# Optimization experiments

Hardware: AMD Instinct MI355X
Metric: run time of the kernel (lower is better)

The kernel has to match this reference:

```python
import jax, jax.numpy as jnp
import numpy as np

KS = 2          # kernel_size
THRESH = 0.0    # conv filter threshold
D = 64          # embed_dim


def setup_inputs() -> dict:
    key = jax.random.key(0)
    k1, k2 = jax.random.split(key, 2)
    x = jax.random.normal(k1, (8, 1, 65, 65), dtype=jnp.float32)
    proj_w = jax.random.normal(k2, (1, D), dtype=jnp.float32) / jnp.sqrt(jnp.float32(D))
    proj_b = jnp.zeros((1,), dtype=jnp.float32)
    return {"x": x, "proj_w": proj_w, "proj_b": proj_b}


def reference(x, proj_w, proj_b):
    B = x.shape[0]
    # non-overlapping stride-1 unfold -> patches (B, KS*KS, H', W')
    patches = jax.lax.conv_general_dilated_patches(x, (KS, KS), (1, 1), 'VALID')
    pat = patches.reshape(B, KS * KS, -1)            # (B, kk, N)
    # Conv.run: one scalar per patch index, shared across the batch
    scalar = jnp.tanh(jnp.mean(pat, axis=(0, 1)) - THRESH)  # (N,)
    N = scalar.shape[0]
    conv_out = jnp.broadcast_to(scalar, (B, N))      # (B, N)
    # np.tile of conv scalar across embed_dim
    embed = jnp.broadcast_to(conv_out[..., None], (B, N, D))  # (B, N, D)
    # rotation/entangle params are identity matrices -> Q = K = V = embed
    scores = jnp.einsum('bnd,bmd->bnm', embed, embed) / jnp.sqrt(jnp.float32(D))
    attn = jax.nn.softmax(scores, axis=-1)           # (B, N, N)
    ctx = jnp.einsum('bnm,bmd->bnd', attn, embed)    # (B, N, D)
    pooled = ctx.mean(axis=1)                        # (B, D)
    out = pooled @ proj_w.T + proj_b                 # (B, 1)
    return out[:, 0]
```

## Files before the change

### kernel.cpp

```cpp
#include <hip/hip_runtime.h>

#define NROW 4096
#define NCOL 4225
#define BATCH 8
#define MAGIC 0x13579BDFu


__device__ __forceinline__ float fast_tanh(float x) {
    float e = __builtin_exp2f(2.885390082f * x);
    return 1.0f - 2.0f / (e + 1.0f);
}

__global__ void __launch_bounds__(1024) k_fused(const float* __restrict__ x,
                                                const float* __restrict__ proj_w,
                                                const float* __restrict__ proj_b,
                                                float* __restrict__ out,
                                                float* __restrict__ partial,
                                                unsigned* __restrict__ flags) {
    __shared__ __align__(16) float cs_sh[NCOL];
    __shared__ __align__(16) float s_sh[NROW];
    __shared__ float c_sh[16];
    const int tid = threadIdx.x;
    const int bid = blockIdx.x;

#pragma unroll
    for (int k = 0; k < 4; ++k) {
        int p = tid + (k << 10);
        float v = 0.0f;
#pragma unroll
        for (int b = 0; b < BATCH; ++b) v += x[b * NCOL + p];
        cs_sh[p] = v;
    }
    if (tid < NCOL - NROW) {
        int p = NROW + tid;
        float v = 0.0f;
#pragma unroll
        for (int b = 0; b < BATCH; ++b) v += x[b * NCOL + p];
        cs_sh[p] = v;
    }
    __syncthreads();

#pragma unroll
    for (int k = 0; k < 4; ++k) {
        int n = tid + (k << 10);
        int i = n >> 6, j = n & 63;
        const float* c = &cs_sh[i * 65 + j];
        s_sh[n] = fast_tanh((c[0] + c[1] + c[65] + c[66]) * (1.0f / 32.0f));
    }
    __syncthreads();

    const int wave = tid >> 6;
    const int lane = tid & 63;
    const int row = (bid << 4) + wave;
    const float t = 8.0f * 1.4426950408889634f * s_sh[row];
    float num = 0.0f, den = 0.0f;
    const float4* s4 = (const float4*)s_sh;
#pragma unroll
    for (int k = 0; k < 16; ++k) {
        float4 sv = s4[lane + (k << 6)];
        float e0 = __builtin_exp2f(t * sv.x);
        float e1 = __builtin_exp2f(t * sv.y);
        float e2 = __builtin_exp2f(t * sv.z);
        float e3 = __builtin_exp2f(t * sv.w);
        num += e0 * sv.x;
        den += e0;
        num += e1 * sv.y;
        den += e1;
        num += e2 * sv.z;
        den += e2;
        num += e3 * sv.w;
        den += e3;
    }
#pragma unroll
    for (int off = 32; off; off >>= 1) {
        num += __shfl_down(num, off, 64);
        den += __shfl_down(den, off, 64);
    }
    if (lane == 0) c_sh[wave] = num / den;
    __syncthreads();

    if (tid == 0) {
        float bs = 0.0f;
#pragma unroll
        for (int r = 0; r < 16; ++r) bs += c_sh[r];
        atomicExch(&partial[bid], bs);
        __threadfence();
        atomicExch(&flags[bid], MAGIC);
    }

    if (bid == 0 && tid < 64) {
        float pw = proj_w[tid];
        float pb = proj_b[0];
#pragma unroll
        for (int q = 0; q < 4; ++q) {
            int i = tid + (q << 6);
            while (atomicAdd(&flags[i], 0u) != MAGIC) __builtin_amdgcn_s_sleep(1);
        }
        __threadfence();
        float acc_c = 0.0f;
#pragma unroll
        for (int q = 0; q < 4; ++q) {
            int i = tid + (q << 6);
            acc_c += atomicAdd(&partial[i], 0.0f);
        }
#pragma unroll
        for (int off = 32; off; off >>= 1) {
            acc_c += __shfl_down(acc_c, off, 64);
            pw    += __shfl_down(pw, off, 64);
        }
        if (tid == 0) {
            float o = (acc_c * (1.0f / (float)NROW)) * pw + pb;
#pragma unroll
            for (int b = 0; b < BATCH; ++b) out[b] = o;
        }
    }
}

extern "C" void kernel_launch(void* const* d_in, const int* in_sizes, int n_in,
                              void* d_out, int out_size, void* d_ws, size_t ws_size,
                              hipStream_t stream) {
    const float* x      = (const float*)d_in[0];
    const float* proj_w = (const float*)d_in[1];
    const float* proj_b = (const float*)d_in[2];
    float* out = (float*)d_out;

    float*    partial = (float*)d_ws;
    unsigned* flags   = (unsigned*)(partial + 256);

    k_fused<<<256, 1024, 0, stream>>>(x, proj_w, proj_b, out, partial, flags);
}
```

Before: 67.84 us.

## Replace in-kernel flag spin synchronisation with a separate final reduction kernel

Splits the fused kernel into a per-row kernel that writes one partial sum per block and a tiny one-wave kernel that reduces the partials and applies the projection. This removes the atomic flag publishing, the fences and the spin-wait in block 0, which also removes the reliance on flags that were never reset between calls. The cost is an extra kernel launch and the dependency gap between the two kernels on the stream.

```diff
diff --git a/kernel.cpp b/kernel.cpp
--- a/kernel.cpp
+++ b/kernel.cpp
@@ -3,7 +3,6 @@
 #define NROW 4096
 #define NCOL 4225
 #define BATCH 8
-#define MAGIC 0x13579BDFu
 
 
 __device__ __forceinline__ float fast_tanh(float x) {
@@ -11,12 +10,8 @@
     return 1.0f - 2.0f / (e + 1.0f);
 }
 
-__global__ void __launch_bounds__(1024) k_fused(const float* __restrict__ x,
-                                                const float* __restrict__ proj_w,
-                                                const float* __restrict__ proj_b,
-                                                float* __restrict__ out,
-                                                float* __restrict__ partial,
-                                                unsigned* __restrict__ flags) {
+__global__ void __launch_bounds__(1024) k_rows(const float* __restrict__ x,
+                                               float* __restrict__ partial) {
     __shared__ __align__(16) float cs_sh[NCOL];
     __shared__ __align__(16) float s_sh[NROW];
     __shared__ float c_sh[16];
@@ -83,36 +78,28 @@
         float bs = 0.0f;
 #pragma unroll
         for (int r = 0; r < 16; ++r) bs += c_sh[r];
-        atomicExch(&partial[bid], bs);
-        __threadfence();
-        atomicExch(&flags[bid], MAGIC);
+        partial[bid] = bs;
     }
+}
 
-    if (bid == 0 && tid < 64) {
-        float pw = proj_w[tid];
-        float pb = proj_b[0];
+__global__ void __launch_bounds__(64) k_final(const float* __restrict__ partial,
+                                              const float* __restrict__ proj_w,
+                                              const float* __restrict__ proj_b,
+                                              float* __restrict__ out) {
+    const int lane = threadIdx.x;
+    float acc = 0.0f;
 #pragma unroll
-        for (int q = 0; q < 4; ++q) {
-            int i = tid + (q << 6);
-            while (atomicAdd(&flags[i], 0u) != MAGIC) __builtin_amdgcn_s_sleep(1);
-        }
-        __threadfence();
-        float acc_c = 0.0f;
+    for (int q = 0; q < 4; ++q) acc += partial[lane + (q << 6)];
+    float pw = proj_w[lane];
 #pragma unroll
-        for (int q = 0; q < 4; ++q) {
-            int i = tid + (q << 6);
-            acc_c += atomicAdd(&partial[i], 0.0f);
-        }
+    for (int off = 32; off; off >>= 1) {
+        acc += __shfl_down(acc, off, 64);
+        pw  += __shfl_down(pw, off, 64);
+    }
+    if (lane == 0) {
+        float o = (acc * (1.0f / (float)NROW)) * pw + proj_b[0];
 #pragma unroll
-        for (int off = 32; off; off >>= 1) {
-            acc_c += __shfl_down(acc_c, off, 64);
-            pw    += __shfl_down(pw, off, 64);
-        }
-        if (tid == 0) {
-            float o = (acc_c * (1.0f / (float)NROW)) * pw + pb;
-#pragma unroll
-            for (int b = 0; b < BATCH; ++b) out[b] = o;
-        }
+        for (int b = 0; b < BATCH; ++b) out[b] = o;
     }
 }
 
@@ -124,8 +111,8 @@
     const float* proj_b = (const float*)d_in[2];
     float* out = (float*)d_out;
 
-    float*    partial = (float*)d_ws;
-    unsigned* flags   = (unsigned*)(partial + 256);
+    float* partial = (float*)d_ws;
 
-    k_fused<<<256, 1024, 0, stream>>>(x, proj_w, proj_b, out, partial, flags);
+    k_rows<<<256, 1024, 0, stream>>>(x, partial);
+    k_final<<<1, 64, 0, stream>>>(partial, proj_w, proj_b, out);
 }
```

New measurement: 64.65 us. -4.7%, faster.
